# Kernel tuning notes

Hardware: AMD Instinct MI355X
Metric: run time of the kernel (lower is better)

The kernel has to match this reference:

```python
import jax, jax.numpy as jnp
import numpy as np

B, N = 2048, 4096

def setup_inputs() -> dict:
    key = jax.random.key(0)
    k1, k2, k3, k4, k5 = jax.random.split(key, 5)
    scale = 1.0 / np.sqrt(N)  # match nn.Linear init scale
    return {
        "t": jnp.zeros((1,), dtype=jnp.float32),
        "y": jax.random.uniform(k1, (B, N), dtype=jnp.float32),
        "W1": jax.random.normal(k2, (N, N), dtype=jnp.float32) * scale,
        "b1": jax.random.normal(k3, (N,), dtype=jnp.float32) * scale,
        "W2": jax.random.normal(k4, (N, N), dtype=jnp.float32) * scale,
        "b2": jax.random.normal(k5, (N,), dtype=jnp.float32) * scale,
    }

def reference(t, y, W1, b1, W2, b2):
    # out = fcc2(fcc1(y)) : two Linear layers (y @ W^T + b)
    h = y @ W1.T + b1            # [B, N]
    out = h @ W2.T + b2          # [B, N]
    # f = ones(N,1) @ y @ out^T  ==  dot(y, out) broadcast over N;
    # dydt = y * (out - dot(y, out))   (replicator equation)
    dot = jnp.sum(y * out, axis=-1, keepdims=True)  # [B, 1]
    return y * (out - dot)       # [B, N]
```

## Files before the change

kernel.cpp:

```cpp
#include <hip/hip_runtime.h>
#include <hip/hip_bf16.h>
#include <stdint.h>

typedef _Float16 f16;
typedef _Float16 f16x4 __attribute__((ext_vector_type(4)));
typedef _Float16 f16x8 __attribute__((ext_vector_type(8)));
typedef float f32x4 __attribute__((ext_vector_type(4)));

#define ASYNC_COPY16(gsrc, ldst)                                                   \
    __builtin_amdgcn_global_load_lds(                                              \
        (__attribute__((address_space(1))) void*)(gsrc),                           \
        (__attribute__((address_space(3))) void*)(ldst), 16, 0, 0)

__global__ __launch_bounds__(256) void cvt_f32_to_f16(const float* __restrict__ in,
                                                      f16* __restrict__ out, int n4) {
    int i = blockIdx.x * 256 + threadIdx.x;
    if (i >= n4) return;
    float4 v = ((const float4*)in)[i];
    f16x4 o;
    o.x = (f16)v.x; o.y = (f16)v.y; o.z = (f16)v.z; o.w = (f16)v.w;
    ((f16x4*)out)[i] = o;
}

__global__ __launch_bounds__(256) void cvt3_f32_to_f16(const float* __restrict__ y,
                                                       const float* __restrict__ W1,
                                                       const float* __restrict__ W2,
                                                       f16* __restrict__ yb,
                                                       f16* __restrict__ w1b,
                                                       f16* __restrict__ w2b,
                                                       int nY4, int nW4) {
    int i = blockIdx.x * 256 + threadIdx.x;
    const float* src;
    f16* dst;
    int off;
    if (i < nY4) {
        src = y; dst = yb; off = i;
    } else if (i < nY4 + nW4) {
        src = W1; dst = w1b; off = i - nY4;
    } else {
        src = W2; dst = w2b; off = i - nY4 - nW4;
        if (off >= nW4) return;
    }
    float4 v = ((const float4*)src)[off];
    f16x4 o;
    o.x = (f16)v.x; o.y = (f16)v.y; o.z = (f16)v.z; o.w = (f16)v.w;
    ((f16x4*)dst)[off] = o;
}

template <int STORE_F16>
__global__ __launch_bounds__(512, 1) void gemm_bt(const f16* __restrict__ A,
                                                  const f16* __restrict__ Bm,
                                                  const float* __restrict__ bias,
                                                  void* __restrict__ Cout,
                                                  int M, int N, int K) {
    constexpr int BM = 128, BN = 256, BK = 64;
    __shared__ __align__(16) f16 sA[3][BM * BK];
    __shared__ __align__(16) f16 sB[3][BN * BK];

    const int tid   = threadIdx.x;
    const int lane  = tid & 63;
    const int wave  = tid >> 6;
    const int waveM = wave >> 2;
    const int waveN = wave & 3;

    const int bm = blockIdx.y * BM;
    const int bn = blockIdx.x * BN;

    const f16* Aptr = A + (size_t)bm * K;
    const f16* Bptr = Bm + (size_t)bn * K;

    const int srow = tid >> 3;
    const int sseg = tid & 7;

    const f16* gA[2];
    const f16* gB[4];
#pragma unroll
    for (int s = 0; s < 2; s++) {
        const int row = s * 64 + srow;
        const int seg = sseg ^ (row & 7);
        gA[s] = Aptr + (size_t)row * K + seg * 8;
    }
#pragma unroll
    for (int s = 0; s < 4; s++) {
        const int row = s * 64 + srow;
        const int seg = sseg ^ (row & 7);
        gB[s] = Bptr + (size_t)row * K + seg * 8;
    }
    const int ldst = tid * 8;

#define STAGE_A(s, buf, k0) ASYNC_COPY16(gA[s] + (k0), &sA[buf][(s)*4096 + ldst])
#define STAGE_B(s, buf, k0) ASYNC_COPY16(gB[s] + (k0), &sB[buf][(s)*4096 + ldst])

    f32x4 acc[4][4] = {};

    const int quad = lane >> 4;
    const int l16  = lane & 15;

    const int iters = K / BK;

#pragma unroll
    for (int s = 0; s < 2; s++) STAGE_A(s, 0, 0);
#pragma unroll
    for (int s = 0; s < 4; s++) STAGE_B(s, 0, 0);
#pragma unroll
    for (int s = 0; s < 2; s++) STAGE_A(s, 1, BK);
#pragma unroll
    for (int s = 0; s < 4; s++) STAGE_B(s, 1, BK);
    asm volatile("s_waitcnt vmcnt(6)" ::: "memory");
    __builtin_amdgcn_s_barrier();

    int cbuf = 0;
    for (int t = 0; t < iters; ++t) {
        const int pbuf = (cbuf >= 1) ? cbuf - 1 : 2;
        const bool st  = (t + 2 < iters);
        const int k0   = (t + 2) * BK;

        {
            f16x8 af[4], bf[4];
#pragma unroll
            for (int mi = 0; mi < 4; mi++) {
                const int row = waveM * 64 + mi * 16 + l16;
                const int seg = (0 * 4 + quad) ^ (row & 7);
                af[mi] = *(const f16x8*)&sA[cbuf][row * BK + seg * 8];
            }
#pragma unroll
            for (int ni = 0; ni < 4; ni++) {
                const int row = waveN * 64 + ni * 16 + l16;
                const int seg = (0 * 4 + quad) ^ (row & 7);
                bf[ni] = *(const f16x8*)&sB[cbuf][row * BK + seg * 8];
            }
            if (st) {
                STAGE_A(0, pbuf, k0);
                STAGE_A(1, pbuf, k0);
                STAGE_B(0, pbuf, k0);
            }
            __builtin_amdgcn_s_barrier();
            asm volatile("s_waitcnt lgkmcnt(0)" ::: "memory");
            __builtin_amdgcn_s_setprio(1);
#pragma unroll
            for (int mi = 0; mi < 4; mi++)
#pragma unroll
                for (int ni = 0; ni < 4; ni++)
                    acc[mi][ni] = __builtin_amdgcn_mfma_f32_16x16x32_f16(af[mi], bf[ni],
                                                                         acc[mi][ni], 0, 0, 0);
            __builtin_amdgcn_s_setprio(0);
            __builtin_amdgcn_s_barrier();
        }

        {
            f16x8 af[4], bf[4];
#pragma unroll
            for (int mi = 0; mi < 4; mi++) {
                const int row = waveM * 64 + mi * 16 + l16;
                const int seg = (1 * 4 + quad) ^ (row & 7);
                af[mi] = *(const f16x8*)&sA[cbuf][row * BK + seg * 8];
            }
#pragma unroll
            for (int ni = 0; ni < 4; ni++) {
                const int row = waveN * 64 + ni * 16 + l16;
                const int seg = (1 * 4 + quad) ^ (row & 7);
                bf[ni] = *(const f16x8*)&sB[cbuf][row * BK + seg * 8];
            }
            if (st) {
                STAGE_B(1, pbuf, k0);
                STAGE_B(2, pbuf, k0);
                STAGE_B(3, pbuf, k0);
            }
            __builtin_amdgcn_s_barrier();
            asm volatile("s_waitcnt lgkmcnt(0)" ::: "memory");
            __builtin_amdgcn_s_setprio(1);
#pragma unroll
            for (int mi = 0; mi < 4; mi++)
#pragma unroll
                for (int ni = 0; ni < 4; ni++)
                    acc[mi][ni] = __builtin_amdgcn_mfma_f32_16x16x32_f16(af[mi], bf[ni],
                                                                         acc[mi][ni], 0, 0, 0);
            __builtin_amdgcn_s_setprio(0);
            if (st) {
                asm volatile("s_waitcnt vmcnt(6)" ::: "memory");
            } else {
                asm volatile("s_waitcnt vmcnt(0)" ::: "memory");
            }
            __builtin_amdgcn_s_barrier();
        }

        cbuf = (cbuf >= 2) ? 0 : cbuf + 1;
    }

#undef STAGE_A
#undef STAGE_B

#pragma unroll
    for (int ni = 0; ni < 4; ni++) {
        const int col = bn + waveN * 64 + ni * 16 + l16;
        const float bv = bias[col];
#pragma unroll
        for (int mi = 0; mi < 4; mi++) {
            const int row0 = bm + waveM * 64 + mi * 16 + quad * 4;
#pragma unroll
            for (int r = 0; r < 4; r++) {
                float v = acc[mi][ni][r] + bv;
                if (STORE_F16)
                    ((f16*)Cout)[(size_t)(row0 + r) * N + col] = (f16)v;
                else
                    ((float*)Cout)[(size_t)(row0 + r) * N + col] = v;
            }
        }
    }
}

__global__ __launch_bounds__(256) void replicator(const float* __restrict__ y,
                                                  float* __restrict__ out, int N) {
    const int row = blockIdx.x;
    const float4* y4 = (const float4*)(y + (size_t)row * N);
    float4* o4 = (float4*)(out + (size_t)row * N);
    const int n4 = N / 4;

    float p = 0.f;
    for (int i = threadIdx.x; i < n4; i += 256) {
        float4 a = y4[i], b = o4[i];
        p += a.x * b.x + a.y * b.y + a.z * b.z + a.w * b.w;
    }
#pragma unroll
    for (int off = 32; off > 0; off >>= 1) p += __shfl_down(p, off, 64);

    __shared__ float sred[4];
    if ((threadIdx.x & 63) == 0) sred[threadIdx.x >> 6] = p;
    __syncthreads();
    const float dot = sred[0] + sred[1] + sred[2] + sred[3];

    for (int i = threadIdx.x; i < n4; i += 256) {
        float4 a = y4[i], b = o4[i];
        float4 r;
        r.x = a.x * (b.x - dot);
        r.y = a.y * (b.y - dot);
        r.z = a.z * (b.z - dot);
        r.w = a.w * (b.w - dot);
        o4[i] = r;
    }
}

extern "C" void kernel_launch(void* const* d_in, const int* in_sizes, int n_in,
                              void* d_out, int out_size, void* d_ws, size_t ws_size,
                              hipStream_t stream) {
    const float* y  = (const float*)d_in[1];
    const float* W1 = (const float*)d_in[2];
    const float* b1 = (const float*)d_in[3];
    const float* W2 = (const float*)d_in[4];
    const float* b2 = (const float*)d_in[5];

    const int N = in_sizes[3];
    const int B = in_sizes[1] / N;
    float* out = (float*)d_out;

    const size_t szY = (size_t)B * N;
    const size_t szW = (size_t)N * N;

    const int yn4 = (int)(szY / 4);
    const int wn4 = (int)(szW / 4);

    dim3 g1(N / 256, B / 128);

    const size_t need_big = (szY + 2 * szW + szY) * sizeof(f16);

    if (ws_size >= need_big) {
        f16* yb  = (f16*)d_ws;
        f16* w1b = yb + szY;
        f16* w2b = w1b + szW;
        f16* hb  = w2b + szW;

        const int tot4 = yn4 + 2 * wn4;
        cvt3_f32_to_f16<<<(tot4 + 255) / 256, 256, 0, stream>>>(y, W1, W2, yb, w1b, w2b,
                                                                yn4, wn4);
        gemm_bt<1><<<g1, 512, 0, stream>>>(yb, w1b, b1, hb, B, N, N);
        gemm_bt<0><<<g1, 512, 0, stream>>>(hb, w2b, b2, out, B, N, N);
    } else {
        f16* yb = (f16*)d_ws;
        f16* wb = yb + szY;
        f16* hb = wb + szW;

        cvt_f32_to_f16<<<yn4 / 256, 256, 0, stream>>>(y, yb, yn4);
        cvt_f32_to_f16<<<wn4 / 256, 256, 0, stream>>>(W1, wb, wn4);
        gemm_bt<1><<<g1, 512, 0, stream>>>(yb, wb, b1, hb, B, N, N);
        cvt_f32_to_f16<<<wn4 / 256, 256, 0, stream>>>(W2, wb, wn4);
        gemm_bt<0><<<g1, 512, 0, stream>>>(hb, wb, b2, out, B, N, N);
    }

    replicator<<<B, 256, 0, stream>>>(y, out, N);
}
```

Baseline: 350.3 us.

## Software-pipeline LDS fragment reads with MFMA quadrants across iterations

Restructures the GEMM main loop so LDS fragment loads for the next quarter-tile are issued while MFMAs on the current quarter run. The last quadrant of each iteration is carried into the next iteration's start, and a tail MFMA batch runs after the loop. Per-iteration barriers drop from four to one, and sched_barrier fences pin the interleaving. The aim is to hide LDS latency and cut barrier stalls, at the cost of more live registers and a more fragile schedule. The swizzle also changes from row&7 to l16&7, which matches because the row bases are multiples of 16.

```diff
diff --git a/kernel.cpp b/kernel.cpp
--- a/kernel.cpp
+++ b/kernel.cpp
@@ -11,6 +11,8 @@
     __builtin_amdgcn_global_load_lds(                                              \
         (__attribute__((address_space(1))) void*)(gsrc),                           \
         (__attribute__((address_space(3))) void*)(ldst), 16, 0, 0)
+
+#define MFMA16(a, b, c) __builtin_amdgcn_mfma_f32_16x16x32_f16((a), (b), (c), 0, 0, 0)
 
 __global__ __launch_bounds__(256) void cvt_f32_to_f16(const float* __restrict__ in,
                                                       f16* __restrict__ out, int n4) {
@@ -98,6 +100,19 @@
 
     const int iters = K / BK;
 
+    int cbuf = 0;
+
+    auto rdA = [&](int mi, int kh) -> f16x8 {
+        const int row = waveM * 64 + mi * 16 + l16;
+        const int seg = (kh * 4 + quad) ^ (l16 & 7);
+        return *(const f16x8*)&sA[cbuf][row * BK + seg * 8];
+    };
+    auto rdB = [&](int ni, int kh) -> f16x8 {
+        const int row = waveN * 64 + ni * 16 + l16;
+        const int seg = (kh * 4 + quad) ^ (l16 & 7);
+        return *(const f16x8*)&sB[cbuf][row * BK + seg * 8];
+    };
+
 #pragma unroll
     for (int s = 0; s < 2; s++) STAGE_A(s, 0, 0);
 #pragma unroll
@@ -109,82 +124,97 @@
     asm volatile("s_waitcnt vmcnt(6)" ::: "memory");
     __builtin_amdgcn_s_barrier();
 
-    int cbuf = 0;
+    f16x8 aP0 = {}, aP1 = {}, bP[4] = {};
+
     for (int t = 0; t < iters; ++t) {
         const int pbuf = (cbuf >= 1) ? cbuf - 1 : 2;
         const bool st  = (t + 2 < iters);
         const int k0   = (t + 2) * BK;
 
-        {
-            f16x8 af[4], bf[4];
-#pragma unroll
-            for (int mi = 0; mi < 4; mi++) {
-                const int row = waveM * 64 + mi * 16 + l16;
-                const int seg = (0 * 4 + quad) ^ (row & 7);
-                af[mi] = *(const f16x8*)&sA[cbuf][row * BK + seg * 8];
+        f16x8 a0[2], b0[4];
+#pragma unroll
+        for (int mi = 0; mi < 2; mi++) a0[mi] = rdA(mi, 0);
+#pragma unroll
+        for (int ni = 0; ni < 4; ni++) b0[ni] = rdB(ni, 0);
+        if (st) {
+            STAGE_A(0, pbuf, k0);
+            STAGE_A(1, pbuf, k0);
+            STAGE_B(0, pbuf, k0);
+        }
+        __builtin_amdgcn_sched_barrier(0);
+
+        if (t > 0) {
+            __builtin_amdgcn_s_setprio(1);
+#pragma unroll
+            for (int ni = 0; ni < 4; ni++) {
+                acc[2][ni] = MFMA16(aP0, bP[ni], acc[2][ni]);
+                acc[3][ni] = MFMA16(aP1, bP[ni], acc[3][ni]);
             }
-#pragma unroll
-            for (int ni = 0; ni < 4; ni++) {
-                const int row = waveN * 64 + ni * 16 + l16;
-                const int seg = (0 * 4 + quad) ^ (row & 7);
-                bf[ni] = *(const f16x8*)&sB[cbuf][row * BK + seg * 8];
-            }
-            if (st) {
-                STAGE_A(0, pbuf, k0);
-                STAGE_A(1, pbuf, k0);
-                STAGE_B(0, pbuf, k0);
-            }
-            __builtin_amdgcn_s_barrier();
-            asm volatile("s_waitcnt lgkmcnt(0)" ::: "memory");
-            __builtin_amdgcn_s_setprio(1);
-#pragma unroll
-            for (int mi = 0; mi < 4; mi++)
-#pragma unroll
-                for (int ni = 0; ni < 4; ni++)
-                    acc[mi][ni] = __builtin_amdgcn_mfma_f32_16x16x32_f16(af[mi], bf[ni],
-                                                                         acc[mi][ni], 0, 0, 0);
             __builtin_amdgcn_s_setprio(0);
-            __builtin_amdgcn_s_barrier();
-        }
-
-        {
-            f16x8 af[4], bf[4];
-#pragma unroll
-            for (int mi = 0; mi < 4; mi++) {
-                const int row = waveM * 64 + mi * 16 + l16;
-                const int seg = (1 * 4 + quad) ^ (row & 7);
-                af[mi] = *(const f16x8*)&sA[cbuf][row * BK + seg * 8];
-            }
-#pragma unroll
-            for (int ni = 0; ni < 4; ni++) {
-                const int row = waveN * 64 + ni * 16 + l16;
-                const int seg = (1 * 4 + quad) ^ (row & 7);
-                bf[ni] = *(const f16x8*)&sB[cbuf][row * BK + seg * 8];
-            }
-            if (st) {
-                STAGE_B(1, pbuf, k0);
-                STAGE_B(2, pbuf, k0);
-                STAGE_B(3, pbuf, k0);
-            }
-            __builtin_amdgcn_s_barrier();
-            asm volatile("s_waitcnt lgkmcnt(0)" ::: "memory");
-            __builtin_amdgcn_s_setprio(1);
-#pragma unroll
-            for (int mi = 0; mi < 4; mi++)
-#pragma unroll
-                for (int ni = 0; ni < 4; ni++)
-                    acc[mi][ni] = __builtin_amdgcn_mfma_f32_16x16x32_f16(af[mi], bf[ni],
-                                                                         acc[mi][ni], 0, 0, 0);
-            __builtin_amdgcn_s_setprio(0);
-            if (st) {
-                asm volatile("s_waitcnt vmcnt(6)" ::: "memory");
-            } else {
-                asm volatile("s_waitcnt vmcnt(0)" ::: "memory");
-            }
-            __builtin_amdgcn_s_barrier();
-        }
+        }
+        __builtin_amdgcn_sched_barrier(0);
+
+        f16x8 a1[2];
+#pragma unroll
+        for (int mi = 0; mi < 2; mi++) a1[mi] = rdA(2 + mi, 0);
+        __builtin_amdgcn_sched_barrier(0);
+
+        __builtin_amdgcn_s_setprio(1);
+#pragma unroll
+        for (int ni = 0; ni < 4; ni++) {
+            acc[0][ni] = MFMA16(a0[0], b0[ni], acc[0][ni]);
+            acc[1][ni] = MFMA16(a0[1], b0[ni], acc[1][ni]);
+        }
+        __builtin_amdgcn_s_setprio(0);
+        __builtin_amdgcn_sched_barrier(0);
+
+        f16x8 a2[2];
+#pragma unroll
+        for (int mi = 0; mi < 2; mi++) a2[mi] = rdA(mi, 1);
+#pragma unroll
+        for (int ni = 0; ni < 4; ni++) bP[ni] = rdB(ni, 1);
+        __builtin_amdgcn_sched_barrier(0);
+
+        __builtin_amdgcn_s_setprio(1);
+#pragma unroll
+        for (int ni = 0; ni < 4; ni++) {
+            acc[2][ni] = MFMA16(a1[0], b0[ni], acc[2][ni]);
+            acc[3][ni] = MFMA16(a1[1], b0[ni], acc[3][ni]);
+        }
+        __builtin_amdgcn_s_setprio(0);
+        __builtin_amdgcn_sched_barrier(0);
+
+        aP0 = rdA(2, 1);
+        aP1 = rdA(3, 1);
+        if (st) {
+            STAGE_B(1, pbuf, k0);
+            STAGE_B(2, pbuf, k0);
+            STAGE_B(3, pbuf, k0);
+        }
+        __builtin_amdgcn_sched_barrier(0);
+
+        __builtin_amdgcn_s_setprio(1);
+#pragma unroll
+        for (int ni = 0; ni < 4; ni++) {
+            acc[0][ni] = MFMA16(a2[0], bP[ni], acc[0][ni]);
+            acc[1][ni] = MFMA16(a2[1], bP[ni], acc[1][ni]);
+        }
+        __builtin_amdgcn_s_setprio(0);
+
+        if (st) {
+            asm volatile("s_waitcnt vmcnt(6) lgkmcnt(0)" ::: "memory");
+        } else {
+            asm volatile("s_waitcnt vmcnt(0) lgkmcnt(0)" ::: "memory");
+        }
+        __builtin_amdgcn_s_barrier();
 
         cbuf = (cbuf >= 2) ? 0 : cbuf + 1;
+    }
+
+#pragma unroll
+    for (int ni = 0; ni < 4; ni++) {
+        acc[2][ni] = MFMA16(aP0, bP[ni], acc[2][ni]);
+        acc[3][ni] = MFMA16(aP1, bP[ni], acc[3][ni]);
     }
 
 #undef STAGE_A
```

Result: no change. 352.8 us (+0.7%).
